# Kernel optimization log

Hardware: AMD Instinct MI355X
Metric: run time of the kernel (lower is better)

## Reference

```python
import itertools
import jax, jax.numpy as jnp
import numpy as np

EPS = 1e-5
B_, P_, N_, HID, DE, DO, NCLS = 256, 32, 60, 64, 32, 32, 2


def _edge_indices(N):
    pairs = [p for p in itertools.product(range(N), range(N)) if p[0] != p[1]]
    recv = np.array([p[0] for p in pairs], dtype=np.int32)
    send = np.array([p[1] for p in pairs], dtype=np.int32)
    return recv, send


def _bn(h, g, b):
    # training-mode BatchNorm1d over 2D [M, C]: stats over dim 0 (biased var)
    m = h.mean(0)
    v = h.var(0)
    return (h - m) * jax.lax.rsqrt(v + EPS) * g + b


def _lin_bn_relu(h, w, bi, g, be):
    return jax.nn.relu(_bn(h @ w.T + bi, g, be))


def setup_inputs() -> dict:
    key = jax.random.key(0)
    ks = iter(jax.random.split(key, 32))
    d = {"x": jax.random.normal(next(ks), (B_, P_, N_), dtype=jnp.float32)}
    d["bnx_g"] = jnp.ones((P_,), jnp.float32)
    d["bnx_b"] = jnp.zeros((P_,), jnp.float32)

    def lin(kw, out_d, in_d):
        return jax.random.normal(kw, (out_d, in_d), jnp.float32) * 0.05

    # fr: 2P -> hid -> hid -> De, each Linear+BN
    for i, (od, idim) in enumerate([(HID, 2 * P_), (HID, HID), (DE, HID)], 1):
        d[f"fr{i}_w"] = lin(next(ks), od, idim)
        d[f"fr{i}_b"] = jnp.zeros((od,), jnp.float32)
        d[f"fr{i}_g"] = jnp.ones((od,), jnp.float32)
        d[f"fr{i}_be"] = jnp.zeros((od,), jnp.float32)
    # fo: P+De -> hid -> hid -> Do
    for i, (od, idim) in enumerate([(HID, P_ + DE), (HID, HID), (DO, HID)], 1):
        d[f"fo{i}_w"] = lin(next(ks), od, idim)
        d[f"fo{i}_b"] = jnp.zeros((od,), jnp.float32)
        d[f"fo{i}_g"] = jnp.ones((od,), jnp.float32)
        d[f"fo{i}_be"] = jnp.zeros((od,), jnp.float32)
    d["fc_w"] = lin(next(ks), NCLS, DO)
    d["fc_b"] = jnp.zeros((NCLS,), jnp.float32)
    return d


def reference(x, bnx_g, bnx_b,
              fr1_w, fr1_b, fr1_g, fr1_be,
              fr2_w, fr2_b, fr2_g, fr2_be,
              fr3_w, fr3_b, fr3_g, fr3_be,
              fo1_w, fo1_b, fo1_g, fo1_be,
              fo2_w, fo2_b, fo2_g, fo2_be,
              fo3_w, fo3_b, fo3_g, fo3_be,
              fc_w, fc_b):
    B, P, N = x.shape
    recv, send = _edge_indices(N)  # static, length Nr = N*(N-1)
    Nr = recv.shape[0]

    # batchnorm_x: BatchNorm1d(P) on [B, P, N] -> stats over (batch, particle)
    m = x.mean((0, 2), keepdims=True)
    v = x.var((0, 2), keepdims=True)
    x = (x - m) * jax.lax.rsqrt(v + EPS) * bnx_g[None, :, None] + bnx_b[None, :, None]

    # edge gather (equivalent to x @ Rr / x @ Rs one-hot matmuls)
    Orr = x[:, :, recv]                 # [B, P, Nr]
    Ors = x[:, :, send]                 # [B, P, Nr]
    Bm = jnp.concatenate([Orr, Ors], axis=1)        # [B, 2P, Nr]
    Bm = Bm.transpose(0, 2, 1).reshape(-1, 2 * P)   # [B*Nr, 2P]

    E = _lin_bn_relu(Bm, fr1_w, fr1_b, fr1_g, fr1_be)
    E = _lin_bn_relu(E, fr2_w, fr2_b, fr2_g, fr2_be)
    E = _lin_bn_relu(E, fr3_w, fr3_b, fr3_g, fr3_be)  # [B*Nr, De]
    E = E.reshape(B, Nr, -1)

    # scatter-add edges to receivers (equivalent to einsum('bij,kj->bik', E^T, Rr))
    Ebar = jnp.zeros((B, N, E.shape[-1]), x.dtype).at[:, recv, :].add(E)  # [B, N, De]

    C = jnp.concatenate([x.transpose(0, 2, 1), Ebar], axis=-1)  # [B, N, P+De]
    C = C.reshape(-1, C.shape[-1])

    O = _lin_bn_relu(C, fo1_w, fo1_b, fo1_g, fo1_be)
    O = _lin_bn_relu(O, fo2_w, fo2_b, fo2_g, fo2_be)
    O = _lin_bn_relu(O, fo3_w, fo3_b, fo3_g, fo3_be)  # [B*N, Do]
    O = O.reshape(B, N, -1)

    pooled = O.sum(axis=1)              # [B, Do]
    return pooled @ fc_w.T + fc_b       # [B, num_classes]
```

## Files before the change

### kernel.cpp

```cpp
#include <hip/hip_runtime.h>

typedef unsigned short ushortT;
typedef _Float16 f16x8 __attribute__((ext_vector_type(8)));
typedef __fp16 fp16v2 __attribute__((ext_vector_type(2)));
typedef __attribute__((ext_vector_type(4))) float f32x4;

constexpr int B_ = 256, P_ = 32, N_ = 60;
constexpr int NE = N_ * (N_ - 1);
constexpr int NETOT = B_ * NE;
constexpr int ROWS = B_ * N_;
constexpr float EPS = 1e-5f;

constexpr size_t F_XT  = 0;
constexpr size_t F_EBAR = F_XT + (size_t)ROWS * 32;
constexpr size_t F_HO1 = F_EBAR + (size_t)ROWS * 32;
constexpr size_t F_HO2 = F_HO1 + (size_t)ROWS * 64;
constexpr size_t F_HO3 = F_HO2 + (size_t)ROWS * 64;
constexpr size_t F_U   = F_HO3 + (size_t)ROWS * 32;
constexpr size_t F_V   = F_U + (size_t)ROWS * 64;
constexpr size_t F_UH  = F_V + (size_t)ROWS * 64;
constexpr size_t F_VH  = F_UH + (size_t)ROWS * 32;
constexpr size_t G_B   = F_VH + (size_t)ROWS * 32;
constexpr size_t G_INS = G_B;
constexpr size_t G_BN1 = G_INS + 8 * 64;
constexpr size_t G_ST2 = G_BN1 + 256 * 128;
constexpr size_t G_ST3 = G_ST2 + 64 * 128;
constexpr size_t G_SO1 = G_ST3 + 64 * 64;
constexpr size_t G_SO2 = G_SO1 + 16 * 128;
constexpr size_t G_SO3 = G_SO2 + 16 * 128;
constexpr size_t G_CNT = 8 * 64 + 256 * 128 + 64 * 128 + 64 * 64 + 16 * 128 + 16 * 128 + 16 * 64;
constexpr size_t F_TOTAL = G_B + G_CNT;

static __device__ __forceinline__ unsigned int cvtpk16(float lo, float hi) {
    union { fp16v2 h; unsigned int u; } r;
    r.h = __builtin_amdgcn_cvt_pkrtz(lo, hi);
    return r.u;
}
static __device__ __forceinline__ unsigned int hadd_relu(unsigned int a, unsigned int b) {
    unsigned int r;
    asm("v_pk_add_f16 %0, %1, %2\n\tv_pk_max_f16 %0, %0, 0"
        : "=v"(r) : "v"(a), "v"(b));
    return r;
}
static __device__ __forceinline__ f16x8 ldf16(const float* __restrict__ p) {
    float4 a = *reinterpret_cast<const float4*>(p);
    float4 b = *reinterpret_cast<const float4*>(p + 4);
    union { unsigned int u[4]; f16x8 v; } r;
    r.u[0] = cvtpk16(a.x, a.y); r.u[1] = cvtpk16(a.z, a.w);
    r.u[2] = cvtpk16(b.x, b.y); r.u[3] = cvtpk16(b.z, b.w);
    return r.v;
}
static __device__ __forceinline__ f16x8 erelu(uint4 uu, uint4 vv, bool ok) {
    union { unsigned int u[4]; f16x8 v; } r;
    r.u[0] = hadd_relu(uu.x, vv.x);
    r.u[1] = hadd_relu(uu.y, vv.y);
    r.u[2] = hadd_relu(uu.z, vv.z);
    r.u[3] = hadd_relu(uu.w, vv.w);
    if (!ok) { r.u[0] = 0u; r.u[1] = 0u; r.u[2] = 0u; r.u[3] = 0u; }
    return r.v;
}

__global__ __launch_bounds__(256) void k0_part(const float* __restrict__ x,
                                               float* __restrict__ ws) {
    int p = blockIdx.x & 31, seg = blockIdx.x >> 5;
    float s = 0.f, q = 0.f;
    for (int idx = threadIdx.x; idx < 32 * N_; idx += 256) {
        int bb = seg * 32 + idx / N_;
        int n = idx - (idx / N_) * N_;
        float v = x[(size_t)(bb * P_ + p) * N_ + n];
        s += v; q += v * v;
    }
    for (int o = 32; o > 0; o >>= 1) { s += __shfl_down(s, o); q += __shfl_down(q, o); }
    __shared__ float rs[4], rq[4];
    int wid = threadIdx.x >> 6, lane = threadIdx.x & 63;
    if (lane == 0) { rs[wid] = s; rq[wid] = q; }
    __syncthreads();
    if (threadIdx.x == 0) {
        s = rs[0] + rs[1] + rs[2] + rs[3];
        q = rq[0] + rq[1] + rq[2] + rq[3];
        float* slot = ws + G_INS + (size_t)seg * 64;
        slot[p] = s;
        slot[32 + p] = q;
    }
}

__global__ __launch_bounds__(256) void k1_uv(const float* __restrict__ x,
                                             const float* __restrict__ w1,
                                             const float* __restrict__ bnx_g,
                                             const float* __restrict__ bnx_b,
                                             float* __restrict__ ws) {
    int b = blockIdx.x;
    __shared__ float xs[P_ * N_];
    __shared__ float w1t[64 * 65];
    __shared__ float sX[32], tX[32];
    __shared__ float rbn[4][5][64];
    const int t = threadIdx.x;
    if (t < 32) {
        float S = 0.f, Q = 0.f;
        #pragma unroll
        for (int s = 0; s < 8; ++s) {
            S += ws[G_INS + (size_t)s * 64 + t];
            Q += ws[G_INS + (size_t)s * 64 + 32 + t];
        }
        float inv = 1.f / (float)(B_ * N_);
        float mean = S * inv;
        float var = Q * inv - mean * mean;
        float sc = bnx_g[t] * rsqrtf(var + EPS);
        sX[t] = sc;
        tX[t] = bnx_b[t] - mean * sc;
    }
    for (int idx = t; idx < 64 * 64; idx += 256) {
        int k = idx >> 6, c = idx & 63;
        w1t[c * 65 + k] = w1[idx];
    }
    __syncthreads();
    for (int idx = t; idx < P_ * N_; idx += 256) {
        int p = idx / N_, n = idx - (idx / N_) * N_;
        xs[idx] = sX[p] * x[(size_t)(b * P_ + p) * N_ + n] + tX[p];
    }
    __syncthreads();
    for (int idx = t; idx < N_ * P_; idx += 256) {
        int n = idx / P_, p = idx - (idx / P_) * P_;
        ws[F_XT + (size_t)(b * N_ + n) * P_ + p] = xs[p * N_ + n];
    }
    const int k = t & 63, ph = t >> 6;
    float wu[32], wv[32];
    #pragma unroll
    for (int p = 0; p < 32; ++p) {
        wu[p] = w1t[p * 65 + k];
        wv[p] = w1t[(32 + p) * 65 + k];
    }
    float su = 0, sv = 0, suu = 0, svv = 0, suv = 0;
    for (int idx = t; idx < N_ * 64; idx += 256) {
        int n = idx >> 6;
        float u = 0.f, v = 0.f;
        #pragma unroll
        for (int p = 0; p < 32; ++p) {
            float xv = xs[p * N_ + n];
            u += xv * wu[p];
            v += xv * wv[p];
        }
        ws[F_U + (size_t)(b * N_ + n) * 64 + k] = u;
        ws[F_V + (size_t)(b * N_ + n) * 64 + k] = v;
        su += u; sv += v; suu += u * u; svv += v * v; suv += u * v;
    }
    rbn[ph][0][k] = su; rbn[ph][1][k] = sv; rbn[ph][2][k] = suu;
    rbn[ph][3][k] = svv; rbn[ph][4][k] = suv;
    __syncthreads();
    if (t < 64) {
        float S_u = 0, S_v = 0, Quu = 0, Qvv = 0, Quv = 0;
        #pragma unroll
        for (int p2 = 0; p2 < 4; ++p2) {
            S_u += rbn[p2][0][t]; S_v += rbn[p2][1][t]; Quu += rbn[p2][2][t];
            Qvv += rbn[p2][3][t]; Quv += rbn[p2][4][t];
        }
        float* slot = ws + G_BN1 + (size_t)b * 128;
        slot[t] = 59.f * (S_u + S_v);
        slot[64 + t] = 59.f * (Quu + Qvv) + 2.f * (S_u * S_v - Quv);
    }
}

__global__ __launch_bounds__(256) void k3b(const float* __restrict__ g,
                                           const float* __restrict__ be,
                                           float* __restrict__ ws) {
    __shared__ float sc[64], sh[64];
    const int t = threadIdx.x;
    if (blockIdx.x < 64 && t < 128) ws[G_ST2 + (size_t)blockIdx.x * 128 + t] = 0.f;
    if (t < 64) {
        float S = 0.f, Q = 0.f;
        for (int s = 0; s < 256; ++s) {
            S += ws[G_BN1 + (size_t)s * 128 + t];
            Q += ws[G_BN1 + (size_t)s * 128 + 64 + t];
        }
        float inv = 1.f / (float)NETOT;
        float mean = S * inv, var = Q * inv - mean * mean;
        float s_ = g[t] * rsqrtf(var + EPS);
        sc[t] = s_;
        sh[t] = be[t] - mean * s_;
    }
    __syncthreads();
    size_t gid = (size_t)blockIdx.x * 256 + t;
    size_t base = gid * 8;
    int k0 = (int)(gid & 7) << 3;
    float4 u0 = *reinterpret_cast<const float4*>(ws + F_U + base);
    float4 u1 = *reinterpret_cast<const float4*>(ws + F_U + base + 4);
    float4 v0 = *reinterpret_cast<const float4*>(ws + F_V + base);
    float4 v1 = *reinterpret_cast<const float4*>(ws + F_V + base + 4);
    uint4 ou, ov;
    ou.x = cvtpk16(sc[k0+0]*u0.x + sh[k0+0], sc[k0+1]*u0.y + sh[k0+1]);
    ou.y = cvtpk16(sc[k0+2]*u0.z + sh[k0+2], sc[k0+3]*u0.w + sh[k0+3]);
    ou.z = cvtpk16(sc[k0+4]*u1.x + sh[k0+4], sc[k0+5]*u1.y + sh[k0+5]);
    ou.w = cvtpk16(sc[k0+6]*u1.z + sh[k0+6], sc[k0+7]*u1.w + sh[k0+7]);
    ov.x = cvtpk16(sc[k0+0]*v0.x, sc[k0+1]*v0.y);
    ov.y = cvtpk16(sc[k0+2]*v0.z, sc[k0+3]*v0.w);
    ov.z = cvtpk16(sc[k0+4]*v1.x, sc[k0+5]*v1.y);
    ov.w = cvtpk16(sc[k0+6]*v1.z, sc[k0+7]*v1.w);
    reinterpret_cast<uint4*>(ws + F_UH)[gid] = ou;
    reinterpret_cast<uint4*>(ws + F_VH)[gid] = ov;
}

template <int STAGE>
__global__ __launch_bounds__(256, 4) void kedge(
    const float* __restrict__ fr2_w, const float* __restrict__ fr3_w,
    const float* __restrict__ g2, const float* __restrict__ be2,
    const float* __restrict__ g3, const float* __restrict__ be3,
    float* __restrict__ ws)
{
    __shared__ __align__(16) ushortT sUVh[75 * 72];
    __shared__ __align__(16) ushortT scrAll[4 * 1024];
    __shared__ float sBN[192];
    __shared__ float red[128];

    const int blk = blockIdx.x;
    const int b = blk >> 2, q = blk & 3;
    const int t = threadIdx.x;
    const int wv = t >> 6, lane = t & 63;
    const int gq = lane >> 4, ln = lane & 15;
    const f32x4 zero = {0.f, 0.f, 0.f, 0.f};

    if constexpr (STAGE == 1) {
        if (blk < 64 && t < 64) ws[G_ST3 + (size_t)blk * 64 + t] = 0.f;
    } else if constexpr (STAGE == 2) {
        if (blk < 16 && t < 128) ws[G_SO1 + (size_t)blk * 128 + t] = 0.f;
    } else {
        if (blk < 16 && t < 128) ws[G_SO2 + (size_t)blk * 128 + t] = 0.f;
    }

    {
        const ushortT* vh = reinterpret_cast<const ushortT*>(ws + F_VH) + (size_t)b * N_ * 64;
        const ushortT* uh = reinterpret_cast<const ushortT*>(ws + F_UH) + (size_t)(b * N_ + q * 15) * 64;
        for (int idx = t; idx < 480; idx += 256) {
            int r = idx >> 3, c = (idx & 7) << 3;
            *reinterpret_cast<uint4*>(&sUVh[r * 72 + c]) =
                *reinterpret_cast<const uint4*>(&vh[(size_t)r * 64 + c]);
        }
        if (t < 120) {
            int r = t >> 3, c = (t & 7) << 3;
            *reinterpret_cast<uint4*>(&sUVh[(60 + r) * 72 + c]) =
                *reinterpret_cast<const uint4*>(&uh[(size_t)r * 64 + c]);
        }
    }
    if constexpr (STAGE >= 2) {
        if (t < 64) {
            float S = 0.f, Q = 0.f;
            for (int s = 0; s < 64; ++s) {
                S += ws[G_ST2 + (size_t)s * 128 + t];
                Q += ws[G_ST2 + (size_t)s * 128 + 64 + t];
            }
            float inv = 1.f / (float)NETOT;
            float m = S * inv, var = Q * inv - m * m;
            float s_ = g2[t] * rsqrtf(var + EPS);
            sBN[t] = s_; sBN[64 + t] = be2[t] - m * s_;
        }
    }
    if constexpr (STAGE == 3) {
        if (t >= 64 && t < 96) {
            int tt = t - 64;
            float S = 0.f, Q = 0.f;
            for (int s = 0; s < 64; ++s) {
                S += ws[G_ST3 + (size_t)s * 64 + tt];
                Q += ws[G_ST3 + (size_t)s * 64 + 32 + tt];
            }
            float inv = 1.f / (float)NETOT;
            float m = S * inv, var = Q * inv - m * m;
            float s_ = g3[tt] * rsqrtf(var + EPS);
            sBN[128 + tt] = s_; sBN[160 + tt] = be3[tt] - m * s_;
        }
    }
    if (t < 128) red[t] = 0.f;

    f16x8 w2f0[4], w2f1[4], w3f0[2], w3f1[2];
    #pragma unroll
    for (int mu = 0; mu < 4; ++mu) {
        w2f0[mu] = ldf16(fr2_w + (size_t)(mu * 16 + ln) * 64 + gq * 8);
        w2f1[mu] = ldf16(fr2_w + (size_t)(mu * 16 + ln) * 64 + 32 + gq * 8);
    }
    if constexpr (STAGE >= 2) {
        #pragma unroll
        for (int nv = 0; nv < 2; ++nv) {
            w3f0[nv] = ldf16(fr3_w + (size_t)(nv * 16 + ln) * 64 + gq * 8);
            w3f1[nv] = ldf16(fr3_w + (size_t)(nv * 16 + ln) * 64 + 32 + gq * 8);
        }
    }
    __syncthreads();

    ushortT* scr = scrAll + wv * 1024;

    if constexpr (STAGE == 1) {
        f32x4 s1s[4] = {zero, zero, zero, zero};
        f32x4 s1q[4] = {zero, zero, zero, zero};
        for (int gi = wv; gi < 15; gi += 4) {
            const int i = q * 15 + gi;
            uint4 uu0 = *reinterpret_cast<const uint4*>(&sUVh[(60 + gi) * 72 + gq * 8]);
            uint4 uu1 = *reinterpret_cast<const uint4*>(&sUVh[(60 + gi) * 72 + 32 + gq * 8]);
            #pragma unroll
            for (int m = 0; m < 4; ++m) {
                int e = (m << 4) + ln;
                int j = e + (e >= i ? 1 : 0);
                uint4 vv0 = *reinterpret_cast<const uint4*>(&sUVh[j * 72 + gq * 8]);
                uint4 vv1 = *reinterpret_cast<const uint4*>(&sUVh[j * 72 + 32 + gq * 8]);
                f16x8 ef0 = erelu(uu0, vv0, e < 59);
                f16x8 ef1 = erelu(uu1, vv1, e < 59);
                #pragma unroll
                for (int mu = 0; mu < 4; ++mu) {
                    f32x4 acc = __builtin_amdgcn_mfma_f32_16x16x32_f16(w2f0[mu], ef0, zero, 0, 0, 0);
                    acc = __builtin_amdgcn_mfma_f32_16x16x32_f16(w2f1[mu], ef1, acc, 0, 0, 0);
                    s1s[mu] += acc;
                    s1q[mu] += acc * acc;
                }
            }
        }
        #pragma unroll
        for (int off = 1; off <= 8; off <<= 1)
            #pragma unroll
            for (int mu = 0; mu < 4; ++mu)
                #pragma unroll
                for (int r = 0; r < 4; ++r) {
                    s1s[mu][r] += __shfl_xor(s1s[mu][r], off);
                    s1q[mu][r] += __shfl_xor(s1q[mu][r], off);
                }
        if (ln == 0) {
            #pragma unroll
            for (int mu = 0; mu < 4; ++mu)
                #pragma unroll
                for (int r = 0; r < 4; ++r) {
                    atomicAdd(&red[mu * 16 + gq * 4 + r], s1s[mu][r]);
                    atomicAdd(&red[64 + mu * 16 + gq * 4 + r], s1q[mu][r]);
                }
        }
        __syncthreads();
        if (t < 128) atomicAdd(ws + G_ST2 + (size_t)(blk & 63) * 128 + t, red[t]);
    } else {
        float st0 = 0.f, st1 = 0.f, st2 = 0.f, st3 = 0.f;
        const float s30 = sBN[128 + ln], s31 = sBN[144 + ln];
        const float t30 = sBN[160 + ln], t31 = sBN[176 + ln];
        for (int gi = wv; gi < 15; gi += 4) {
            const int i = q * 15 + gi;
            uint4 uu0 = *reinterpret_cast<const uint4*>(&sUVh[(60 + gi) * 72 + gq * 8]);
            uint4 uu1 = *reinterpret_cast<const uint4*>(&sUVh[(60 + gi) * 72 + 32 + gq * 8]);
            float es0 = 0.f, es1 = 0.f;
            #pragma unroll
            for (int m = 0; m < 4; ++m) {
                int e = (m << 4) + ln;
                int j = e + (e >= i ? 1 : 0);
                uint4 vv0 = *reinterpret_cast<const uint4*>(&sUVh[j * 72 + gq * 8]);
                uint4 vv1 = *reinterpret_cast<const uint4*>(&sUVh[j * 72 + 32 + gq * 8]);
                const bool eok = e < 59;
                f16x8 ef0 = erelu(uu0, vv0, eok);
                f16x8 ef1 = erelu(uu1, vv1, eok);
                f32x4 ac[4];
                #pragma unroll
                for (int mu = 0; mu < 4; ++mu) {
                    ac[mu] = __builtin_amdgcn_mfma_f32_16x16x32_f16(w2f0[mu], ef0, zero, 0, 0, 0);
                    ac[mu] = __builtin_amdgcn_mfma_f32_16x16x32_f16(w2f1[mu], ef1, ac[mu], 0, 0, 0);
                }
                #pragma unroll
                for (int mu = 0; mu < 4; ++mu) {
                    int fb = mu * 16 + (gq << 2);
                    float4 sc2 = *reinterpret_cast<const float4*>(sBN + fb);
                    float4 sh2 = *reinterpret_cast<const float4*>(sBN + 64 + fb);
                    unsigned int pk0 = cvtpk16(fmaxf(0.f, sc2.x * ac[mu][0] + sh2.x),
                                               fmaxf(0.f, sc2.y * ac[mu][1] + sh2.y));
                    unsigned int pk1 = cvtpk16(fmaxf(0.f, sc2.z * ac[mu][2] + sh2.z),
                                               fmaxf(0.f, sc2.w * ac[mu][3] + sh2.w));
                    if (!eok) { pk0 = 0u; pk1 = 0u; }
                    int lp = ln + ((((mu << 1) + (gq >> 1)) & 3) << 4);
                    int off = ((mu >> 1) << 9) + (lp << 3) + ((gq & 1) << 2);
                    uint2 pr; pr.x = pk0; pr.y = pk1;
                    *reinterpret_cast<uint2*>(&scr[off]) = pr;
                }
                __threadfence_block();
                union { uint4 q4; f16x8 v; } ea0, ea1;
                ea0.q4 = *reinterpret_cast<const uint4*>(&scr[lane << 3]);
                ea1.q4 = *reinterpret_cast<const uint4*>(&scr[512 + (lane << 3)]);
                f32x4 a30 = __builtin_amdgcn_mfma_f32_16x16x32_f16(ea0.v, w3f0[0], zero, 0, 0, 0);
                a30 = __builtin_amdgcn_mfma_f32_16x16x32_f16(ea1.v, w3f1[0], a30, 0, 0, 0);
                f32x4 a31 = __builtin_amdgcn_mfma_f32_16x16x32_f16(ea0.v, w3f0[1], zero, 0, 0, 0);
                a31 = __builtin_amdgcn_mfma_f32_16x16x32_f16(ea1.v, w3f1[1], a31, 0, 0, 0);
                if constexpr (STAGE == 2) {
                    #pragma unroll
                    for (int r = 0; r < 4; ++r) {
                        st0 += a30[r]; st1 += a30[r] * a30[r];
                        st2 += a31[r]; st3 += a31[r] * a31[r];
                    }
                } else {
                    #pragma unroll
                    for (int r = 0; r < 4; ++r) {
                        if ((m << 4) + (gq << 2) + r < 59) {
                            es0 += fmaxf(0.f, s30 * a30[r] + t30);
                            es1 += fmaxf(0.f, s31 * a31[r] + t31);
                        }
                    }
                }
            }
            if constexpr (STAGE == 3) {
                es0 += __shfl_xor(es0, 16); es0 += __shfl_xor(es0, 32);
                es1 += __shfl_xor(es1, 16); es1 += __shfl_xor(es1, 32);
                if (lane < 16) {
                    ws[F_EBAR + (size_t)(b * N_ + i) * 32 + ln] = es0;
                    ws[F_EBAR + (size_t)(b * N_ + i) * 32 + 16 + ln] = es1;
                }
            }
        }
        if constexpr (STAGE == 2) {
            st0 += __shfl_xor(st0, 16); st0 += __shfl_xor(st0, 32);
            st1 += __shfl_xor(st1, 16); st1 += __shfl_xor(st1, 32);
            st2 += __shfl_xor(st2, 16); st2 += __shfl_xor(st2, 32);
            st3 += __shfl_xor(st3, 16); st3 += __shfl_xor(st3, 32);
            if (lane < 16) {
                atomicAdd(&red[ln], st0);      atomicAdd(&red[16 + ln], st2);
                atomicAdd(&red[32 + ln], st1); atomicAdd(&red[48 + ln], st3);
            }
            __syncthreads();
            if (t < 64) atomicAdd(ws + G_ST3 + (size_t)(blk & 63) * 64 + t, red[t]);
        }
    }
}

template <int OUT, int FIN>
__global__ __launch_bounds__(256) void kobj(const float* __restrict__ srcA,
                                            const float* __restrict__ srcB,
                                            const float* __restrict__ statIn,
                                            const float* __restrict__ gP,
                                            const float* __restrict__ beP,
                                            const float* __restrict__ W,
                                            float* __restrict__ outp,
                                            float* __restrict__ statOut,
                                            float* __restrict__ zeroPtr,
                                            int zeroCnt) {
    constexpr int TRN = (OUT == 64) ? 16 : 32;
    constexpr int RB = 4 * TRN;
    constexpr int SP = RB + 4;
    constexpr int WP = OUT + 4;
    __shared__ __align__(16) float sinT[64 * SP];
    __shared__ __align__(16) float swt[64 * WP];
    __shared__ float sAct[128];
    const int t = threadIdx.x;
    const int row0 = blockIdx.x * RB;
    if (zeroPtr && (int)blockIdx.x < 16 && t < zeroCnt)
        zeroPtr[(size_t)blockIdx.x * zeroCnt + t] = 0.f;
    if (FIN > 0 && t < 64) {
        float S = 0.f, Q = 0.f;
        #pragma unroll
        for (int s = 0; s < 16; ++s) {
            S += statIn[(size_t)s * 128 + t];
            Q += statIn[(size_t)s * 128 + 64 + t];
        }
        float inv = 1.f / (float)ROWS;
        float m = S * inv, var = Q * inv - m * m;
        float sc = gP[t] * rsqrtf(var + EPS);
        sAct[t] = sc; sAct[64 + t] = beP[t] - m * sc;
    }
    __syncthreads();
    for (int idx = t; idx < RB * 64; idx += 256) {
        int r = idx % RB, k = idx / RB;
        float v;
        if (srcB) {
            v = (k < 32) ? srcA[(size_t)(row0 + r) * 32 + k]
                         : srcB[(size_t)(row0 + r) * 32 + (k - 32)];
        } else {
            v = srcA[(size_t)(row0 + r) * 64 + k];
        }
        if (FIN > 0) v = fmaxf(0.f, sAct[k] * v + sAct[64 + k]);
        sinT[k * SP + r] = v;
    }
    for (int idx = t; idx < OUT * 64; idx += 256) {
        int o = idx >> 6, k = idx & 63;
        swt[k * WP + o] = W[idx];
    }
    __syncthreads();
    const int tr = t % TRN, to = t / TRN;
    const int r0 = tr * 4, o0 = to * 4;
    float acc[4][4];
    #pragma unroll
    for (int a = 0; a < 4; ++a)
        #pragma unroll
        for (int c = 0; c < 4; ++c) acc[a][c] = 0.f;
    #pragma unroll 8
    for (int k = 0; k < 64; ++k) {
        float4 a4 = *reinterpret_cast<const float4*>(sinT + k * SP + r0);
        float4 w4 = *reinterpret_cast<const float4*>(swt + k * WP + o0);
        float av[4] = {a4.x, a4.y, a4.z, a4.w};
        float wv[4] = {w4.x, w4.y, w4.z, w4.w};
        #pragma unroll
        for (int a = 0; a < 4; ++a)
            #pragma unroll
            for (int c = 0; c < 4; ++c) acc[a][c] += av[a] * wv[c];
    }
    float lsum[4] = {0.f, 0.f, 0.f, 0.f}, lsq[4] = {0.f, 0.f, 0.f, 0.f};
    #pragma unroll
    for (int a = 0; a < 4; ++a) {
        float4 res;
        res.x = acc[a][0]; res.y = acc[a][1]; res.z = acc[a][2]; res.w = acc[a][3];
        #pragma unroll
        for (int c = 0; c < 4; ++c) { lsum[c] += acc[a][c]; lsq[c] += acc[a][c] * acc[a][c]; }
        *reinterpret_cast<float4*>(outp + (size_t)(row0 + r0 + a) * OUT + o0) = res;
    }
    #pragma unroll
    for (int o = TRN / 2; o >= 1; o >>= 1) {
        #pragma unroll
        for (int c = 0; c < 4; ++c) {
            lsum[c] += __shfl_down(lsum[c], o, TRN);
            lsq[c]  += __shfl_down(lsq[c], o, TRN);
        }
    }
    if (tr == 0) {
        float* so = statOut + (size_t)(blockIdx.x & 15) * (2 * OUT);
        #pragma unroll
        for (int c = 0; c < 4; ++c) {
            atomicAdd(so + o0 + c, lsum[c]);
            atomicAdd(so + OUT + o0 + c, lsq[c]);
        }
    }
}

__global__ __launch_bounds__(64) void k15_final(const float* __restrict__ g,
                                                const float* __restrict__ be,
                                                const float* __restrict__ fcw,
                                                const float* __restrict__ fcb,
                                                float* __restrict__ ws,
                                                float* __restrict__ out) {
    __shared__ float sc3s[32], sh3s[32];
    int b = blockIdx.x, t = threadIdx.x;
    if (t < 32) {
        float S = 0.f, Q = 0.f;
        #pragma unroll
        for (int s = 0; s < 16; ++s) {
            S += ws[G_SO3 + (size_t)s * 64 + t];
            Q += ws[G_SO3 + (size_t)s * 64 + 32 + t];
        }
        float inv = 1.f / (float)ROWS;
        float m = S * inv, var = Q * inv - m * m;
        float sc = g[t] * rsqrtf(var + EPS);
        sc3s[t] = sc; sh3s[t] = be[t] - m * sc;
    }
    __syncthreads();
    int f = t & 31, h = t >> 5;
    float sc = sc3s[f], sh = sh3s[f];
    float acc = 0.f;
    for (int n = h; n < N_; n += 2) {
        float v = ws[F_HO3 + (size_t)(b * N_ + n) * 32 + f];
        acc += fmaxf(0.f, sc * v + sh);
    }
    acc += __shfl_down(acc, 32);
    float p0 = acc * fcw[f];
    float p1 = acc * fcw[32 + f];
    #pragma unroll
    for (int o = 16; o >= 1; o >>= 1) {
        p0 += __shfl_xor(p0, o);
        p1 += __shfl_xor(p1, o);
    }
    if (t == 0) {
        out[b * 2 + 0] = p0 + fcb[0];
        out[b * 2 + 1] = p1 + fcb[1];
    }
}

extern "C" void kernel_launch(void* const* d_in, const int* in_sizes, int n_in,
                              void* d_out, int out_size, void* d_ws, size_t ws_size,
                              hipStream_t stream) {
    const float* x      = (const float*)d_in[0];
    const float* bnx_g  = (const float*)d_in[1];
    const float* bnx_b  = (const float*)d_in[2];
    const float* fr1_w  = (const float*)d_in[3];
    const float* fr1_g  = (const float*)d_in[5];
    const float* fr1_be = (const float*)d_in[6];
    const float* fr2_w  = (const float*)d_in[7];
    const float* fr2_g  = (const float*)d_in[9];
    const float* fr2_be = (const float*)d_in[10];
    const float* fr3_w  = (const float*)d_in[11];
    const float* fr3_g  = (const float*)d_in[13];
    const float* fr3_be = (const float*)d_in[14];
    const float* fo1_w  = (const float*)d_in[15];
    const float* fo1_g  = (const float*)d_in[17];
    const float* fo1_be = (const float*)d_in[18];
    const float* fo2_w  = (const float*)d_in[19];
    const float* fo2_g  = (const float*)d_in[21];
    const float* fo2_be = (const float*)d_in[22];
    const float* fo3_w  = (const float*)d_in[23];
    const float* fo3_g  = (const float*)d_in[25];
    const float* fo3_be = (const float*)d_in[26];
    const float* fc_w   = (const float*)d_in[27];
    const float* fc_b   = (const float*)d_in[28];

    float* ws = (float*)d_ws;
    float* out = (float*)d_out;
    if (ws_size < F_TOTAL * sizeof(float)) return;

    k0_part<<<256, 256, 0, stream>>>(x, ws);
    k1_uv<<<B_, 256, 0, stream>>>(x, fr1_w, bnx_g, bnx_b, ws);
    k3b<<<480, 256, 0, stream>>>(fr1_g, fr1_be, ws);
    kedge<1><<<B_ * 4, 256, 0, stream>>>(fr2_w, fr3_w, fr2_g, fr2_be, fr3_g, fr3_be, ws);
    kedge<2><<<B_ * 4, 256, 0, stream>>>(fr2_w, fr3_w, fr2_g, fr2_be, fr3_g, fr3_be, ws);
    kedge<3><<<B_ * 4, 256, 0, stream>>>(fr2_w, fr3_w, fr2_g, fr2_be, fr3_g, fr3_be, ws);
    kobj<64, 0><<<ROWS / 64, 256, 0, stream>>>(ws + F_XT, ws + F_EBAR, nullptr, nullptr, nullptr,
                                               fo1_w, ws + F_HO1, ws + G_SO1, ws + G_SO3, 64);
    kobj<64, 64><<<ROWS / 64, 256, 0, stream>>>(ws + F_HO1, nullptr, ws + G_SO1, fo1_g, fo1_be,
                                                fo2_w, ws + F_HO2, ws + G_SO2, nullptr, 0);
    kobj<32, 64><<<ROWS / 128, 256, 0, stream>>>(ws + F_HO2, nullptr, ws + G_SO2, fo2_g, fo2_be,
                                                 fo3_w, ws + F_HO3, ws + G_SO3, nullptr, 0);
    k15_final<<<B_, 64, 0, stream>>>(fo3_g, fo3_be, fc_w, fc_b, ws, out);
}
```

Measured before the change: 145.4 us.

## Materialize fr3 pre-activations in fp16 and replace third edge recompute with scatter kernel

Instead of recomputing the fr2/fr3 edge MLP a third time to apply the final BatchNorm and scatter-add, the second edge pass now stores fr3 outputs as fp16 in a new workspace buffer while also accumulating statistics. A new kernel finalizes BN3 stats, applies scale/shift and ReLU, and sums edges per receiver. This trades redundant MFMA compute for a large extra write and read of edge activations, with narrow 16-bit scattered stores and added fp16 rounding before normalization.

Measured after the change: 142.7 us. No clear change (-1.9%).

```diff
diff --git a/kernel.cpp b/kernel.cpp
--- a/kernel.cpp
+++ b/kernel.cpp
@@ -20,7 +20,8 @@
 constexpr size_t F_V   = F_U + (size_t)ROWS * 64;
 constexpr size_t F_UH  = F_V + (size_t)ROWS * 64;
 constexpr size_t F_VH  = F_UH + (size_t)ROWS * 32;
-constexpr size_t G_B   = F_VH + (size_t)ROWS * 32;
+constexpr size_t F_H3  = F_VH + (size_t)ROWS * 32;
+constexpr size_t G_B   = F_H3 + (size_t)NETOT * 16;
 constexpr size_t G_INS = G_B;
 constexpr size_t G_BN1 = G_INS + 8 * 64;
 constexpr size_t G_ST2 = G_BN1 + 256 * 128;
@@ -203,12 +204,11 @@
 __global__ __launch_bounds__(256, 4) void kedge(
     const float* __restrict__ fr2_w, const float* __restrict__ fr3_w,
     const float* __restrict__ g2, const float* __restrict__ be2,
-    const float* __restrict__ g3, const float* __restrict__ be3,
     float* __restrict__ ws)
 {
     __shared__ __align__(16) ushortT sUVh[75 * 72];
     __shared__ __align__(16) ushortT scrAll[4 * 1024];
-    __shared__ float sBN[192];
+    __shared__ float sBN[128];
     __shared__ float red[128];
 
     const int blk = blockIdx.x;
@@ -220,10 +220,8 @@
 
     if constexpr (STAGE == 1) {
         if (blk < 64 && t < 64) ws[G_ST3 + (size_t)blk * 64 + t] = 0.f;
-    } else if constexpr (STAGE == 2) {
+    } else {
         if (blk < 16 && t < 128) ws[G_SO1 + (size_t)blk * 128 + t] = 0.f;
-    } else {
-        if (blk < 16 && t < 128) ws[G_SO2 + (size_t)blk * 128 + t] = 0.f;
     }
 
     {
@@ -240,7 +238,7 @@
                 *reinterpret_cast<const uint4*>(&uh[(size_t)r * 64 + c]);
         }
     }
-    if constexpr (STAGE >= 2) {
+    if constexpr (STAGE == 2) {
         if (t < 64) {
             float S = 0.f, Q = 0.f;
             for (int s = 0; s < 64; ++s) {
@@ -253,20 +251,6 @@
             sBN[t] = s_; sBN[64 + t] = be2[t] - m * s_;
         }
     }
-    if constexpr (STAGE == 3) {
-        if (t >= 64 && t < 96) {
-            int tt = t - 64;
-            float S = 0.f, Q = 0.f;
-            for (int s = 0; s < 64; ++s) {
-                S += ws[G_ST3 + (size_t)s * 64 + tt];
-                Q += ws[G_ST3 + (size_t)s * 64 + 32 + tt];
-            }
-            float inv = 1.f / (float)NETOT;
-            float m = S * inv, var = Q * inv - m * m;
-            float s_ = g3[tt] * rsqrtf(var + EPS);
-            sBN[128 + tt] = s_; sBN[160 + tt] = be3[tt] - m * s_;
-        }
-    }
     if (t < 128) red[t] = 0.f;
 
     f16x8 w2f0[4], w2f1[4], w3f0[2], w3f1[2];
@@ -275,7 +259,7 @@
         w2f0[mu] = ldf16(fr2_w + (size_t)(mu * 16 + ln) * 64 + gq * 8);
         w2f1[mu] = ldf16(fr2_w + (size_t)(mu * 16 + ln) * 64 + 32 + gq * 8);
     }
-    if constexpr (STAGE >= 2) {
+    if constexpr (STAGE == 2) {
         #pragma unroll
         for (int nv = 0; nv < 2; ++nv) {
             w3f0[nv] = ldf16(fr3_w + (size_t)(nv * 16 + ln) * 64 + gq * 8);
@@ -332,13 +316,12 @@
         if (t < 128) atomicAdd(ws + G_ST2 + (size_t)(blk & 63) * 128 + t, red[t]);
     } else {
         float st0 = 0.f, st1 = 0.f, st2 = 0.f, st3 = 0.f;
-        const float s30 = sBN[128 + ln], s31 = sBN[144 + ln];
-        const float t30 = sBN[160 + ln], t31 = sBN[176 + ln];
+        ushortT* __restrict__ h3p = reinterpret_cast<ushortT*>(ws + F_H3);
         for (int gi = wv; gi < 15; gi += 4) {
             const int i = q * 15 + gi;
+            const size_t ebase = ((size_t)b * NE + (size_t)i * 59) * 32;
             uint4 uu0 = *reinterpret_cast<const uint4*>(&sUVh[(60 + gi) * 72 + gq * 8]);
             uint4 uu1 = *reinterpret_cast<const uint4*>(&sUVh[(60 + gi) * 72 + 32 + gq * 8]);
-            float es0 = 0.f, es1 = 0.f;
             #pragma unroll
             for (int m = 0; m < 4; ++m) {
                 int e = (m << 4) + ln;
@@ -377,43 +360,72 @@
                 a30 = __builtin_amdgcn_mfma_f32_16x16x32_f16(ea1.v, w3f1[0], a30, 0, 0, 0);
                 f32x4 a31 = __builtin_amdgcn_mfma_f32_16x16x32_f16(ea0.v, w3f0[1], zero, 0, 0, 0);
                 a31 = __builtin_amdgcn_mfma_f32_16x16x32_f16(ea1.v, w3f1[1], a31, 0, 0, 0);
-                if constexpr (STAGE == 2) {
-                    #pragma unroll
-                    for (int r = 0; r < 4; ++r) {
-                        st0 += a30[r]; st1 += a30[r] * a30[r];
-                        st2 += a31[r]; st3 += a31[r] * a31[r];
-                    }
-                } else {
-                    #pragma unroll
-                    for (int r = 0; r < 4; ++r) {
-                        if ((m << 4) + (gq << 2) + r < 59) {
-                            es0 += fmaxf(0.f, s30 * a30[r] + t30);
-                            es1 += fmaxf(0.f, s31 * a31[r] + t31);
-                        }
+                #pragma unroll
+                for (int r = 0; r < 4; ++r) {
+                    st0 += a30[r]; st1 += a30[r] * a30[r];
+                    st2 += a31[r]; st3 += a31[r] * a31[r];
+                    int el = (m << 4) + (gq << 2) + r;
+                    if (el < 59) {
+                        size_t rb = ebase + (size_t)el * 32;
+                        h3p[rb + ln] = (ushortT)(cvtpk16(a30[r], 0.f) & 0xffffu);
+                        h3p[rb + 16 + ln] = (ushortT)(cvtpk16(a31[r], 0.f) & 0xffffu);
                     }
                 }
             }
-            if constexpr (STAGE == 3) {
-                es0 += __shfl_xor(es0, 16); es0 += __shfl_xor(es0, 32);
-                es1 += __shfl_xor(es1, 16); es1 += __shfl_xor(es1, 32);
-                if (lane < 16) {
-                    ws[F_EBAR + (size_t)(b * N_ + i) * 32 + ln] = es0;
-                    ws[F_EBAR + (size_t)(b * N_ + i) * 32 + 16 + ln] = es1;
-                }
-            }
-        }
-        if constexpr (STAGE == 2) {
-            st0 += __shfl_xor(st0, 16); st0 += __shfl_xor(st0, 32);
-            st1 += __shfl_xor(st1, 16); st1 += __shfl_xor(st1, 32);
-            st2 += __shfl_xor(st2, 16); st2 += __shfl_xor(st2, 32);
-            st3 += __shfl_xor(st3, 16); st3 += __shfl_xor(st3, 32);
-            if (lane < 16) {
-                atomicAdd(&red[ln], st0);      atomicAdd(&red[16 + ln], st2);
-                atomicAdd(&red[32 + ln], st1); atomicAdd(&red[48 + ln], st3);
-            }
-            __syncthreads();
-            if (t < 64) atomicAdd(ws + G_ST3 + (size_t)(blk & 63) * 64 + t, red[t]);
-        }
+        }
+        st0 += __shfl_xor(st0, 16); st0 += __shfl_xor(st0, 32);
+        st1 += __shfl_xor(st1, 16); st1 += __shfl_xor(st1, 32);
+        st2 += __shfl_xor(st2, 16); st2 += __shfl_xor(st2, 32);
+        st3 += __shfl_xor(st3, 16); st3 += __shfl_xor(st3, 32);
+        if (lane < 16) {
+            atomicAdd(&red[ln], st0);      atomicAdd(&red[16 + ln], st2);
+            atomicAdd(&red[32 + ln], st1); atomicAdd(&red[48 + ln], st3);
+        }
+        __syncthreads();
+        if (t < 64) atomicAdd(ws + G_ST3 + (size_t)(blk & 63) * 64 + t, red[t]);
+    }
+}
+
+__global__ __launch_bounds__(256) void k8_scatter(const float* __restrict__ g3,
+                                                  const float* __restrict__ be3,
+                                                  float* __restrict__ ws) {
+    __shared__ float sc3[32], sh3[32];
+    const int t = threadIdx.x;
+    if ((int)blockIdx.x < 16 && t < 128)
+        ws[G_SO2 + (size_t)blockIdx.x * 128 + t] = 0.f;
+    if (t < 32) {
+        float S = 0.f, Q = 0.f;
+        for (int s = 0; s < 64; ++s) {
+            S += ws[G_ST3 + (size_t)s * 64 + t];
+            Q += ws[G_ST3 + (size_t)s * 64 + 32 + t];
+        }
+        float inv = 1.f / (float)NETOT;
+        float m = S * inv, var = Q * inv - m * m;
+        float sc = g3[t] * rsqrtf(var + EPS);
+        sc3[t] = sc; sh3[t] = be3[t] - m * sc;
+    }
+    __syncthreads();
+    const int wv = t >> 6, lane = t & 63;
+    const int fp = lane & 15, h = lane >> 4;
+    const int grp = blockIdx.x * 4 + wv;
+    const int b = grp / N_, i = grp - b * N_;
+    const unsigned int* __restrict__ h3u =
+        reinterpret_cast<const unsigned int*>(ws + F_H3) + ((size_t)b * NE + (size_t)i * 59) * 16;
+    const int f0 = fp * 2;
+    const float s0 = sc3[f0], s1 = sc3[f0 + 1];
+    const float t0 = sh3[f0], t1 = sh3[f0 + 1];
+    float a0 = 0.f, a1 = 0.f;
+    for (int r = h; r < 59; r += 4) {
+        union { unsigned int u; __fp16 hh[2]; } v;
+        v.u = h3u[(size_t)r * 16 + fp];
+        a0 += fmaxf(0.f, s0 * (float)v.hh[0] + t0);
+        a1 += fmaxf(0.f, s1 * (float)v.hh[1] + t1);
+    }
+    a0 += __shfl_xor(a0, 16); a0 += __shfl_xor(a0, 32);
+    a1 += __shfl_xor(a1, 16); a1 += __shfl_xor(a1, 32);
+    if (h == 0) {
+        float2 r2; r2.x = a0; r2.y = a1;
+        *reinterpret_cast<float2*>(ws + F_EBAR + (size_t)grp * 32 + f0) = r2;
     }
 }
 
@@ -590,9 +602,9 @@
     k0_part<<<256, 256, 0, stream>>>(x, ws);
     k1_uv<<<B_, 256, 0, stream>>>(x, fr1_w, bnx_g, bnx_b, ws);
     k3b<<<480, 256, 0, stream>>>(fr1_g, fr1_be, ws);
-    kedge<1><<<B_ * 4, 256, 0, stream>>>(fr2_w, fr3_w, fr2_g, fr2_be, fr3_g, fr3_be, ws);
-    kedge<2><<<B_ * 4, 256, 0, stream>>>(fr2_w, fr3_w, fr2_g, fr2_be, fr3_g, fr3_be, ws);
-    kedge<3><<<B_ * 4, 256, 0, stream>>>(fr2_w, fr3_w, fr2_g, fr2_be, fr3_g, fr3_be, ws);
+    kedge<1><<<B_ * 4, 256, 0, stream>>>(fr2_w, fr3_w, fr2_g, fr2_be, ws);
+    kedge<2><<<B_ * 4, 256, 0, stream>>>(fr2_w, fr3_w, fr2_g, fr2_be, ws);
+    k8_scatter<<<ROWS / 4, 256, 0, stream>>>(fr3_g, fr3_be, ws);
     kobj<64, 0><<<ROWS / 64, 256, 0, stream>>>(ws + F_XT, ws + F_EBAR, nullptr, nullptr, nullptr,
                                                fo1_w, ws + F_HO1, ws + G_SO1, ws + G_SO3, 64);
     kobj<64, 64><<<ROWS / 64, 256, 0, stream>>>(ws + F_HO1, nullptr, ws + G_SO1, fo1_g, fo1_be,
```
